# Optimization experiments

Measured on AMD Instinct MI355X. Metric: run time of the kernel, lower is better.

The kernel has to match this reference:

```python
import jax, jax.numpy as jnp
import numpy as np

B, S, D, H = 2, 2048, 2048, 16
DH = D // H            # 128 head dim
QP = D // 2            # 1024 compressed q dim
KVP = (2 * D) // 3     # 1365 compressed kv dim
RD = DH // 2           # 64 rope dim
ND = DH // 2           # 64 nope dim
FF = 4 * D
THETA = 10000.0


def _ln(x, w, b, eps=1e-5):
    m = jnp.mean(x, -1, keepdims=True)
    v = jnp.mean((x - m) ** 2, -1, keepdims=True)
    return (x - m) * jax.lax.rsqrt(v + eps) * w + b


def _rotate_half(x):
    x1, x2 = jnp.split(x, 2, axis=-1)
    return jnp.concatenate([-x2, x1], axis=-1)


def setup_inputs() -> dict:
    key = jax.random.key(0)
    ks = jax.random.split(key, 9)
    rn = lambda k, shp, s: (s * jax.random.normal(k, shp)).astype(jnp.float32)
    return {
        'x': jax.random.normal(ks[0], (B, S, D), jnp.float32),
        'attn_norm_w': jnp.ones((D,), jnp.float32), 'attn_norm_b': jnp.zeros((D,), jnp.float32),
        'W_dq': rn(ks[1], (D, QP), 0.01),
        'q_ln_w': jnp.ones((QP,), jnp.float32), 'q_ln_b': jnp.zeros((QP,), jnp.float32),
        'W_uq': rn(ks[2], (QP, D), 0.01),
        'W_dkv': rn(ks[3], (D, KVP + RD), 0.01),
        'kv_ln_w': jnp.ones((KVP,), jnp.float32), 'kv_ln_b': jnp.zeros((KVP,), jnp.float32),
        'W_ukv': rn(ks[4], (KVP, D + H * ND), 0.01),
        'W_o': rn(ks[5], (D, D), 0.01),
        'ff_norm_w': jnp.ones((D,), jnp.float32), 'ff_norm_b': jnp.zeros((D,), jnp.float32),
        'W1': rn(ks[6], (D, FF), 0.02), 'b1': jnp.zeros((FF,), jnp.float32),
        'W2': rn(ks[7], (FF, D), 0.02), 'b2': jnp.zeros((D,), jnp.float32),
    }


def reference(x, attn_norm_w, attn_norm_b, W_dq, q_ln_w, q_ln_b, W_uq, W_dkv,
              kv_ln_w, kv_ln_b, W_ukv, W_o, ff_norm_w, ff_norm_b, W1, b1, W2, b2):
    # ---- pre-LN attention ----
    h = _ln(x, attn_norm_w, attn_norm_b)
    # Q path: down-proj, LN, up-proj
    cq = _ln(h @ W_dq, q_ln_w, q_ln_b)                      # [B,S,QP]
    Q = (cq @ W_uq).reshape(B, S, H, DH).transpose(0, 2, 1, 3)  # [B,H,S,DH]
    Qn, Qr = Q[..., :ND], Q[..., ND:]
    # RoPE tables: emb [S, DH/2]; take first RD/2 freqs, tile -> [1,1,S,RD]
    pos = jnp.arange(S, dtype=jnp.float32)
    freqs = 1.0 / (THETA ** (jnp.arange(0, DH, 2, dtype=jnp.float32) / DH))
    emb = pos[:, None] * freqs[None, :]
    cos = jnp.tile(jnp.cos(emb)[:, :RD // 2], (1, 2))[None, None]
    sin = jnp.tile(jnp.sin(emb)[:, :RD // 2], (1, 2))[None, None]
    Qr = Qr * cos + _rotate_half(Qr) * sin
    # KV path: joint down-proj, split latent / shared rope key
    ckv = h @ W_dkv                                          # [B,S,KVP+RD]
    kv_lora, k_rope = ckv[..., :KVP], ckv[..., KVP:]
    kv_lora = _ln(kv_lora, kv_ln_w, kv_ln_b)
    KV = (kv_lora @ W_ukv).reshape(B, S, H, DH + ND).transpose(0, 2, 1, 3)
    K, V = KV[..., :ND], KV[..., ND:]                        # K [B,H,S,ND], V [B,H,S,DH]
    Kr = k_rope[:, None]                                     # [B,1,S,RD] shared across heads
    Kr = Kr * cos + _rotate_half(Kr) * sin
    Kr = jnp.broadcast_to(Kr, (B, H, S, RD))
    q = jnp.concatenate([Qn, Qr], -1)                        # [B,H,S,DH]
    k = jnp.concatenate([K, Kr], -1)                         # [B,H,S,DH]
    scores = jnp.einsum('bhqd,bhkd->bhqk', q, k) / jnp.sqrt(jnp.float32(DH))
    mask = jnp.tril(jnp.ones((S, S), bool))
    scores = jnp.where(mask, scores, jnp.finfo(scores.dtype).min)
    attn = jax.nn.softmax(scores, axis=-1)
    o = jnp.einsum('bhqk,bhkd->bhqd', attn, V).transpose(0, 2, 1, 3).reshape(B, S, D)
    o = o @ W_o.T
    x = x + o  # dropout is identity at eval
    # ---- pre-LN MLP ----
    r = x
    h = _ln(x, ff_norm_w, ff_norm_b)
    h = jax.nn.gelu(h @ W1 + b1, approximate=False) @ W2 + b2
    return r + h, ckv
```

## Files before the change

kernel.cpp:

```cpp
#include <hip/hip_runtime.h>
#include <hip/hip_bf16.h>
#include <math.h>

#define B_ 2
#define S_ 2048
#define D_ 2048
#define H_ 16
#define DH_ 128
#define QP_ 1024
#define KVP_ 1365
#define RD_ 64
#define ND_ 64
#define FF_ 8192
#define T_ (B_*S_)
#define CKW_ (KVP_+RD_)
#define KVW_ 3072
#define KVP_PAD 1408
#define CKW_PAD 1536

typedef __attribute__((ext_vector_type(8))) short short8;
typedef __attribute__((ext_vector_type(4))) short sh4;
typedef __attribute__((ext_vector_type(4))) float floatx4;

__device__ __forceinline__ void gload_lds16(const __hip_bfloat16* g, __hip_bfloat16* l) {
    __builtin_amdgcn_global_load_lds((const __attribute__((address_space(1))) void*)g,
                                     (__attribute__((address_space(3))) void*)l, 16, 0, 0);
}
__device__ __forceinline__ short f2bs(float f) {
    __hip_bfloat16 h = __float2bfloat16(f);
    return *reinterpret_cast<short*>(&h);
}
__device__ __forceinline__ int sw(int row, int g) { return row * 64 + ((g ^ (row & 7)) << 3); }

__device__ __forceinline__ float fast_gelu(float v) {
    float x = v * 0.70710678118654752f;
    float ax = fabsf(x);
    float t = __builtin_amdgcn_rcpf(1.f + 0.3275911f * ax);
    float y = t * (0.254829592f + t * (-0.284496736f + t * (1.421413741f + t * (-1.453152027f + t * 1.061405429f))));
    float e = __expf(-ax * ax);
    float erfv = 1.f - y * e;
    erfv = copysignf(erfv, x);
    return 0.5f * v * (1.f + erfv);
}

__global__ __launch_bounds__(256) void ln_bf16(const float* __restrict__ in, int in_stride,
                                               const float* __restrict__ w, const float* __restrict__ bb,
                                               __hip_bfloat16* __restrict__ out, int out_stride, int N)
{
    int row = blockIdx.x;
    const float* ip = in + (size_t)row * in_stride;
    __hip_bfloat16* op = out + (size_t)row * out_stride;
    int tid = threadIdx.x;
    __shared__ float s1[256], s2[256];
    float sum = 0.f, sq = 0.f;
    bool vec = (((in_stride | N | out_stride) & 3) == 0);
    if (vec) {
        const float4* ip4 = (const float4*)ip;
        int n4 = N >> 2;
        for (int i = tid; i < n4; i += 256) {
            float4 v = ip4[i];
            sum += v.x + v.y + v.z + v.w;
            sq  += v.x * v.x + v.y * v.y + v.z * v.z + v.w * v.w;
        }
        s1[tid] = sum; s2[tid] = sq; __syncthreads();
        for (int s = 128; s > 0; s >>= 1) {
            if (tid < s) { s1[tid] += s1[tid + s]; s2[tid] += s2[tid + s]; }
            __syncthreads();
        }
        float mean = s1[0] / N;
        float var  = s2[0] / N - mean * mean;
        float rstd = rsqrtf(var + 1e-5f);
        const float4* w4 = (const float4*)w;
        const float4* b4 = (const float4*)bb;
        for (int i = tid; i < n4; i += 256) {
            float4 v = ip4[i], wv = w4[i], bv = b4[i];
            sh4 o;
            o[0] = f2bs((v.x - mean) * rstd * wv.x + bv.x);
            o[1] = f2bs((v.y - mean) * rstd * wv.y + bv.y);
            o[2] = f2bs((v.z - mean) * rstd * wv.z + bv.z);
            o[3] = f2bs((v.w - mean) * rstd * wv.w + bv.w);
            *(sh4*)&op[i * 4] = o;
        }
    } else {
        for (int i = tid; i < N; i += 256) { float v = ip[i]; sum += v; sq += v * v; }
        s1[tid] = sum; s2[tid] = sq; __syncthreads();
        for (int s = 128; s > 0; s >>= 1) {
            if (tid < s) { s1[tid] += s1[tid + s]; s2[tid] += s2[tid + s]; }
            __syncthreads();
        }
        float mean = s1[0] / N;
        float var  = s2[0] / N - mean * mean;
        float rstd = rsqrtf(var + 1e-5f);
        for (int i = tid; i < N; i += 256) {
            float v = ip[i];
            op[i] = __float2bfloat16((v - mean) * rstd * w[i] + bb[i]);
        }
    }
    for (int i = N + tid; i < out_stride; i += 256) op[i] = __float2bfloat16(0.f);
}

__global__ __launch_bounds__(256) void transpose_cvt(const float* __restrict__ W, __hip_bfloat16* __restrict__ Wt,
                                                     int K, int N, int Kp)
{
    __shared__ float t[32][33];
    int k0 = blockIdx.x * 32, n0 = blockIdx.y * 32;
    int tx = threadIdx.x & 31, ty = threadIdx.x >> 5;
    for (int r = ty; r < 32; r += 8) {
        int k = k0 + r, n = n0 + tx;
        t[r][tx] = (k < K && n < N) ? W[(size_t)k * N + n] : 0.f;
    }
    __syncthreads();
    for (int r = ty; r < 32; r += 8) {
        int n = n0 + r, k = k0 + tx;
        Wt[(size_t)n * Kp + k] = __float2bfloat16(t[tx][r]);
    }
}

__global__ __launch_bounds__(256) void cvt_bf16(const float* __restrict__ in, __hip_bfloat16* __restrict__ out, int n)
{
    int i = blockIdx.x * 256 + threadIdx.x;
    if (i < n) out[i] = __float2bfloat16(in[i]);
}

template<int EPI, typename CT>
__global__ __launch_bounds__(256) void gemm_bf16(const __hip_bfloat16* __restrict__ A,
                                                 const __hip_bfloat16* __restrict__ Bt,
                                                 CT* __restrict__ C, int M, int N, int Kp, int ldc,
                                                 const float* __restrict__ bias,
                                                 const float* __restrict__ resid)
{
    __shared__ __hip_bfloat16 As[128 * 64];
    __shared__ __hip_bfloat16 Bs[128 * 64];
    int tid = threadIdx.x;
    int gx = gridDim.x;
    int nwg = gx * gridDim.y;
    int o = blockIdx.y * gx + blockIdx.x;
    int sId = ((nwg & 7) == 0) ? ((o & 7) * (nwg >> 3) + (o >> 3)) : o;
    int bm = (sId / gx) * 128;
    int bn = (sId % gx) * 128;
    int wid = tid >> 6, lane = tid & 63;
    int wm = (wid >> 1) * 64, wn = (wid & 1) * 64;
    int lrow = lane & 15;
    int quad = lane >> 4;

    floatx4 acc[4][4];
    #pragma unroll
    for (int i = 0; i < 4; ++i)
        #pragma unroll
        for (int j = 0; j < 4; ++j)
            acc[i][j] = (floatx4){0.f, 0.f, 0.f, 0.f};

    for (int k0 = 0; k0 < Kp; k0 += 64) {
        #pragma unroll
        for (int it = 0; it < 4; ++it) {
            int chunk = it * 256 + tid;
            int row = chunk >> 3, g = chunk & 7;
            int col = (g ^ (row & 7)) << 3;
            gload_lds16(A + (size_t)(bm + row) * Kp + k0 + col, &As[chunk * 8]);
        }
        #pragma unroll
        for (int it = 0; it < 4; ++it) {
            int chunk = it * 256 + tid;
            int row = chunk >> 3, g = chunk & 7;
            int col = (g ^ (row & 7)) << 3;
            gload_lds16(Bt + (size_t)(bn + row) * Kp + k0 + col, &Bs[chunk * 8]);
        }
        __syncthreads();
        #pragma unroll
        for (int kk = 0; kk < 2; ++kk) {
            short8 a[4], b[4];
            #pragma unroll
            for (int i = 0; i < 4; ++i)
                a[i] = *(const short8*)&As[sw(wm + i * 16 + lrow, kk * 4 + quad)];
            #pragma unroll
            for (int j = 0; j < 4; ++j)
                b[j] = *(const short8*)&Bs[sw(wn + j * 16 + lrow, kk * 4 + quad)];
            #pragma unroll
            for (int i = 0; i < 4; ++i)
                #pragma unroll
                for (int j = 0; j < 4; ++j)
                    acc[i][j] = __builtin_amdgcn_mfma_f32_16x16x32_bf16(a[i], b[j], acc[i][j], 0, 0, 0);
        }
        __syncthreads();
    }

    int cq4 = quad * 4;
    #pragma unroll
    for (int i = 0; i < 4; ++i) {
        #pragma unroll
        for (int j = 0; j < 4; ++j) {
            int col = bn + wn + j * 16 + lrow;
            if (col >= N) continue;
            #pragma unroll
            for (int r = 0; r < 4; ++r) {
                int rowg = bm + wm + i * 16 + cq4 + r;
                float v = acc[i][j][r];
                size_t idx = (size_t)rowg * ldc + col;
                if (EPI == 1) v += resid[idx];
                if (EPI == 2) { v += bias[col]; v = fast_gelu(v); }
                if (EPI == 3) { v += bias[col]; v += ((const float*)C)[idx]; }
                C[idx] = (CT)v;
            }
        }
    }
}

#define BARP() __builtin_amdgcn_s_barrier()
#define SCBP() __builtin_amdgcn_sched_barrier(0)
#define GATEP(nw) asm volatile("s_waitcnt vmcnt(" #nw ")" ::: "memory")

template<int EPI, typename CT>
__global__ __launch_bounds__(512, 1) void gemm_pp(const __hip_bfloat16* __restrict__ A,
                                                  const __hip_bfloat16* __restrict__ Bt,
                                                  CT* __restrict__ C, int M, int N, int Kp, int ldc,
                                                  const float* __restrict__ bias,
                                                  const float* __restrict__ resid)
{
    __shared__ __hip_bfloat16 As[3][16384];
    __shared__ __hip_bfloat16 Bs[3][8192];

    int tid = threadIdx.x;
    int wid = tid >> 6, lane = tid & 63;
    int lrow = lane & 15, quad = lane >> 4;
    int awm = (wid >> 1) * 64;
    int bwn = (wid & 1) * 64;

    int gx = gridDim.x;
    int nwg = gx * gridDim.y;
    int o = blockIdx.y * gx + blockIdx.x;
    int q8 = nwg >> 3, r8 = nwg & 7;
    int xcd = o & 7, oi = o >> 3;
    int s = (xcd < r8 ? xcd * (q8 + 1) : r8 * (q8 + 1) + (xcd - r8) * q8) + oi;
    int bm = (s / gx) * 256, bn = (s % gx) * 128;

    const __hip_bfloat16* Abm = A  + (size_t)bm * Kp;
    const __hip_bfloat16* Bbn = Bt + (size_t)bn * Kp;

    int drow = tid >> 3;
    int csw  = ((tid & 7) ^ (drow & 7)) << 3;
    int ldst = tid * 8;

#define PSTAGE_A(k0v, dst) do { \
    gload_lds16(Abm + (size_t)drow * Kp + (k0v) + csw,         (dst) + ldst); \
    gload_lds16(Abm + (size_t)(drow + 64) * Kp + (k0v) + csw,  (dst) + 4096 + ldst); \
    gload_lds16(Abm + (size_t)(drow + 128) * Kp + (k0v) + csw, (dst) + 8192 + ldst); \
    gload_lds16(Abm + (size_t)(drow + 192) * Kp + (k0v) + csw, (dst) + 12288 + ldst); \
  } while (0)
#define PSTAGE_B(k0v, dst) do { \
    gload_lds16(Bbn + (size_t)drow * Kp + (k0v) + csw,        (dst) + ldst); \
    gload_lds16(Bbn + (size_t)(drow + 64) * Kp + (k0v) + csw, (dst) + 4096 + ldst); \
  } while (0)

    int k0off = ((quad       ^ (lrow & 7)) << 3);
    int k1off = (((4 + quad) ^ (lrow & 7)) << 3);

    short8 af0[4], af1[4], bf0[4], bf1[4];
    floatx4 acc[4][4];
    #pragma unroll
    for (int m = 0; m < 4; ++m)
        #pragma unroll
        for (int n = 0; n < 4; ++n)
            acc[m][n] = (floatx4){0.f, 0.f, 0.f, 0.f};

#define PREAD(bufA, bufB, dA, dB, koff) do { \
    _Pragma("unroll") \
    for (int m = 0; m < 4; ++m) \
      dA[m] = *(const short8*)((bufA) + (awm + m * 16 + lrow) * 64 + (koff)); \
    _Pragma("unroll") \
    for (int n = 0; n < 4; ++n) \
      dB[n] = *(const short8*)((bufB) + (bwn + n * 16 + lrow) * 64 + (koff)); \
  } while (0)

#define PMFMA(fa, fb) do { \
    __builtin_amdgcn_s_setprio(1); \
    _Pragma("unroll") \
    for (int m = 0; m < 4; ++m) \
      _Pragma("unroll") \
      for (int n = 0; n < 4; ++n) \
        acc[m][n] = __builtin_amdgcn_mfma_f32_16x16x32_bf16(fa[m], fb[n], acc[m][n], 0, 0, 0); \
    __builtin_amdgcn_s_setprio(0); \
  } while (0)

    __hip_bfloat16 *aC = &As[0][0], *aN = &As[1][0], *aS = &As[2][0];
    __hip_bfloat16 *bC = &Bs[0][0], *bN = &Bs[1][0], *bS = &Bs[2][0];

    int NT = Kp >> 6;

    PSTAGE_A(0, aC);  PSTAGE_B(0, bC);
    PSTAGE_A(64, aN); PSTAGE_B(64, bN);
    GATEP(6); SCBP(); BARP(); SCBP();
    PREAD(aC, bC, af0, bf0, k0off);

    #pragma unroll 1
    for (int t = 0; t < NT; ++t) {
        int ks = ((t + 2 < NT) ? t + 2 : NT - 1) << 6;
        PSTAGE_A(ks, aS); PSTAGE_B(ks, bS);
        PREAD(aC, bC, af1, bf1, k1off);
        PMFMA(af0, bf0);
        GATEP(6); SCBP(); BARP(); SCBP();
        PREAD(aN, bN, af0, bf0, k0off);
        PMFMA(af1, bf1);
        SCBP(); BARP(); SCBP();
        __hip_bfloat16* ta = aC; aC = aN; aN = aS; aS = ta;
        __hip_bfloat16* tb = bC; bC = bN; bN = bS; bS = tb;
    }
    asm volatile("s_waitcnt vmcnt(0)" ::: "memory");

    int cq4 = quad * 4;
    #pragma unroll
    for (int m = 0; m < 4; ++m) {
        int rowg = bm + awm + m * 16 + cq4;
        #pragma unroll
        for (int n = 0; n < 4; ++n) {
            int col = bn + bwn + n * 16 + lrow;
            #pragma unroll
            for (int r = 0; r < 4; ++r) {
                float v = acc[m][n][r];
                size_t idx = (size_t)(rowg + r) * ldc + col;
                if (EPI == 1) v += resid[idx];
                if (EPI == 2) { v += bias[col]; v = fast_gelu(v); }
                if (EPI == 3) { v += bias[col]; v += ((const float*)C)[idx]; }
                C[idx] = (CT)v;
            }
        }
    }
#undef PSTAGE_A
#undef PSTAGE_B
#undef PREAD
#undef PMFMA
}

__global__ __launch_bounds__(256) void rope_q_kernel(float* __restrict__ Q)
{
    int idx = blockIdx.x * 256 + threadIdx.x;
    int i = idx & 31;
    int h = (idx >> 5) & (H_ - 1);
    int t = idx >> 9;
    float f = expf(-(float)i * (9.210340371976184f / 64.0f));
    float ang = (float)(t & (S_ - 1)) * f;
    float sv, cv; sincosf(ang, &sv, &cv);
    float* p = Q + (size_t)t * D_ + h * DH_ + ND_;
    float u = p[i], v = p[i + 32];
    p[i]      = u * cv - v * sv;
    p[i + 32] = v * cv + u * sv;
}

__global__ __launch_bounds__(256) void rope_kr_bf(const float* __restrict__ ckv, __hip_bfloat16* __restrict__ kr)
{
    int idx = blockIdx.x * 256 + threadIdx.x;
    int i = idx & 31;
    int t = idx >> 5;
    float f = expf(-(float)i * (9.210340371976184f / 64.0f));
    float ang = (float)(t & (S_ - 1)) * f;
    float sv, cv; sincosf(ang, &sv, &cv);
    const float* src = ckv + (size_t)t * CKW_ + KVP_;
    float u = src[i], v = src[i + 32];
    kr[(size_t)t * RD_ + i]      = __float2bfloat16(u * cv - v * sv);
    kr[(size_t)t * RD_ + i + 32] = __float2bfloat16(v * cv + u * sv);
}

__global__ __launch_bounds__(256) void vt_pack(const __hip_bfloat16* __restrict__ kvu,
                                               __hip_bfloat16* __restrict__ Vt)
{
    int bh = blockIdx.y; int b = bh >> 4, h = bh & 15;
    int v = threadIdx.x & 127;
    int tg = blockIdx.x * 2 + (threadIdx.x >> 7);
    int t0 = tg * 8;
    short8 o;
    #pragma unroll
    for (int j = 0; j < 8; ++j) {
        __hip_bfloat16 e = kvu[(size_t)(b * S_ + t0 + j) * KVW_ + h * 192 + 64 + v];
        o[j] = *reinterpret_cast<short*>(&e);
    }
    *(short8*)&Vt[((size_t)bh * 128 + v) * S_ + t0] = o;
}

__global__ __launch_bounds__(256) void attn_mfma(const float* __restrict__ Q,
                                                 const __hip_bfloat16* __restrict__ KVU,
                                                 const __hip_bfloat16* __restrict__ KR,
                                                 const __hip_bfloat16* __restrict__ VT,
                                                 __hip_bfloat16* __restrict__ O)
{
    __shared__ __hip_bfloat16 Kls[64 * 64];
    __shared__ __hip_bfloat16 Krls[64 * 64];
    __shared__ __hip_bfloat16 Vls[128 * 64];
    __shared__ __hip_bfloat16 Pls[4 * 32 * 64];

    int tid = threadIdx.x, wid = tid >> 6, lane = tid & 63;
    int lrow = lane & 15, quad = lane >> 4;
    int kq8 = quad * 8;
    int o = blockIdx.y * 16 + blockIdx.x;
    int sId = (o & 7) * 64 + (o >> 3);
    int qtile = 15 - (sId & 15);
    int bh = sId >> 4;
    int b = bh >> 4, h = bh & 15;
    int q0 = qtile * 128, wq = wid * 32;

    const float scale = 0.08838834764831845f;

    short8 bq[2][2], bqr[2][2];
    #pragma unroll
    for (int n = 0; n < 2; ++n) {
        const float* qrow = Q + (size_t)(b * S_ + q0 + wq + n * 16 + lrow) * D_ + h * DH_;
        #pragma unroll
        for (int s = 0; s < 2; ++s) {
            int base = s * 32 + kq8;
            #pragma unroll
            for (int j = 0; j < 8; ++j) {
                bq[n][s][j]  = f2bs(qrow[base + j] * scale);
                bqr[n][s][j] = f2bs(qrow[64 + base + j] * scale);
            }
        }
    }

    float mstate[2] = {-INFINITY, -INFINITY};
    float lstate[2] = {0.f, 0.f};
    floatx4 acco[8][2];
    #pragma unroll
    for (int vt = 0; vt < 8; ++vt)
        #pragma unroll
        for (int n = 0; n < 2; ++n)
            acco[vt][n] = (floatx4){0.f, 0.f, 0.f, 0.f};

    int nk = qtile * 2 + 2;
    int qmax_w = q0 + wq + 31;

    for (int kt = 0; kt < nk; ++kt) {
        int k0 = kt * 64;
        #pragma unroll
        for (int it = 0; it < 2; ++it) {
            int c = it * 256 + tid;
            int row = c >> 3, g = c & 7;
            int col = ((g ^ (row & 7)) << 3);
            gload_lds16(KVU + (size_t)(b * S_ + k0 + row) * KVW_ + h * 192 + col, &Kls[c * 8]);
            gload_lds16(KR + (size_t)(b * S_ + k0 + row) * RD_ + col, &Krls[c * 8]);
        }
        #pragma unroll
        for (int it = 0; it < 4; ++it) {
            int c = it * 256 + tid;
            int row = c >> 3, g = c & 7;
            int col = ((g ^ (row & 7)) << 3);
            gload_lds16(VT + ((size_t)bh * 128 + row) * S_ + k0 + col, &Vls[c * 8]);
        }
        __syncthreads();

        if (k0 <= qmax_w) {
            floatx4 sacc[4][2];
            #pragma unroll
            for (int m = 0; m < 4; ++m)
                #pragma unroll
                for (int n = 0; n < 2; ++n)
                    sacc[m][n] = (floatx4){0.f, 0.f, 0.f, 0.f};
            #pragma unroll
            for (int m = 0; m < 4; ++m) {
                short8 ak[2], akr[2];
                #pragma unroll
                for (int s = 0; s < 2; ++s) {
                    ak[s]  = *(const short8*)&Kls[sw(m * 16 + lrow, s * 4 + quad)];
                    akr[s] = *(const short8*)&Krls[sw(m * 16 + lrow, s * 4 + quad)];
                }
                #pragma unroll
                for (int n = 0; n < 2; ++n)
                    #pragma unroll
                    for (int s = 0; s < 2; ++s) {
                        sacc[m][n] = __builtin_amdgcn_mfma_f32_16x16x32_bf16(ak[s],  bq[n][s],  sacc[m][n], 0, 0, 0);
                        sacc[m][n] = __builtin_amdgcn_mfma_f32_16x16x32_bf16(akr[s], bqr[n][s], sacc[m][n], 0, 0, 0);
                    }
            }
            #pragma unroll
            for (int n = 0; n < 2; ++n) {
                int qg = q0 + wq + n * 16 + lrow;
                float tmax = -INFINITY;
                #pragma unroll
                for (int m = 0; m < 4; ++m)
                    #pragma unroll
                    for (int r = 0; r < 4; ++r) {
                        int kg = k0 + m * 16 + quad * 4 + r;
                        if (kg > qg) sacc[m][n][r] = -1e30f;
                        tmax = fmaxf(tmax, sacc[m][n][r]);
                    }
                tmax = fmaxf(tmax, __shfl_xor(tmax, 16));
                tmax = fmaxf(tmax, __shfl_xor(tmax, 32));
                float mnew = fmaxf(mstate[n], tmax);
                float alpha = __expf(mstate[n] - mnew);
                mstate[n] = mnew;
                float ps = 0.f;
                #pragma unroll
                for (int m = 0; m < 4; ++m) {
                    sh4 pk;
                    #pragma unroll
                    for (int r = 0; r < 4; ++r) {
                        float p = __expf(sacc[m][n][r] - mnew);
                        ps += p;
                        pk[r] = f2bs(p);
                    }
                    int qloc = n * 16 + lrow;
                    int off = wid * 2048 + qloc * 64 + (((m * 2 + (quad >> 1)) ^ (lrow & 7)) << 3) + ((quad & 1) << 2);
                    *(sh4*)&Pls[off] = pk;
                }
                ps += __shfl_xor(ps, 16);
                ps += __shfl_xor(ps, 32);
                lstate[n] = lstate[n] * alpha + ps;
                #pragma unroll
                for (int vt = 0; vt < 8; ++vt)
                    #pragma unroll
                    for (int r = 0; r < 4; ++r)
                        acco[vt][n][r] *= alpha;
            }
            short8 bp[2][2];
            #pragma unroll
            for (int n = 0; n < 2; ++n)
                #pragma unroll
                for (int s = 0; s < 2; ++s)
                    bp[n][s] = *(const short8*)&Pls[wid * 2048 + sw(n * 16 + lrow, s * 4 + quad)];
            #pragma unroll
            for (int vt = 0; vt < 8; ++vt) {
                short8 av[2];
                #pragma unroll
                for (int s = 0; s < 2; ++s)
                    av[s] = *(const short8*)&Vls[sw(vt * 16 + lrow, s * 4 + quad)];
                #pragma unroll
                for (int n = 0; n < 2; ++n)
                    #pragma unroll
                    for (int s = 0; s < 2; ++s)
                        acco[vt][n] = __builtin_amdgcn_mfma_f32_16x16x32_bf16(av[s], bp[n][s], acco[vt][n], 0, 0, 0);
            }
        }
        __syncthreads();
    }

    #pragma unroll
    for (int n = 0; n < 2; ++n) {
        float inv = 1.0f / lstate[n];
        int tok = b * S_ + q0 + wq + n * 16 + lrow;
        #pragma unroll
        for (int vt = 0; vt < 8; ++vt) {
            sh4 o4;
            #pragma unroll
            for (int r = 0; r < 4; ++r) o4[r] = f2bs(acco[vt][n][r] * inv);
            *(sh4*)&O[(size_t)tok * D_ + h * DH_ + vt * 16 + quad * 4] = o4;
        }
    }
}

extern "C" void kernel_launch(void* const* d_in, const int* in_sizes, int n_in,
                              void* d_out, int out_size, void* d_ws, size_t ws_size,
                              hipStream_t stream)
{
    const float* x     = (const float*)d_in[0];
    const float* anw   = (const float*)d_in[1];
    const float* anb   = (const float*)d_in[2];
    const float* W_dq  = (const float*)d_in[3];
    const float* qlw   = (const float*)d_in[4];
    const float* qlb   = (const float*)d_in[5];
    const float* W_uq  = (const float*)d_in[6];
    const float* W_dkv = (const float*)d_in[7];
    const float* kvlw  = (const float*)d_in[8];
    const float* kvlb  = (const float*)d_in[9];
    const float* W_ukv = (const float*)d_in[10];
    const float* W_o   = (const float*)d_in[11];
    const float* fnw   = (const float*)d_in[12];
    const float* fnb   = (const float*)d_in[13];
    const float* W1    = (const float*)d_in[14];
    const float* b1    = (const float*)d_in[15];
    const float* W2    = (const float*)d_in[16];
    const float* b2    = (const float*)d_in[17];

    float* out0 = (float*)d_out;
    float* ckv  = out0 + (size_t)T_ * D_;

    float* ws = (float*)d_ws;
    float* Q  = ws;
    float* cq = Q + (size_t)T_ * D_;
    __hip_bfloat16* kvu_bf = (__hip_bfloat16*)(cq + (size_t)T_ * QP_);
    __hip_bfloat16* kr_bf  = kvu_bf + (size_t)T_ * KVW_;
    __hip_bfloat16* Vt     = kr_bf + (size_t)T_ * RD_;
    __hip_bfloat16* h_bf   = Vt + (size_t)T_ * D_;
    __hip_bfloat16* cq_bf  = h_bf + (size_t)T_ * D_;
    __hip_bfloat16* kvl_bf = cq_bf + (size_t)T_ * QP_;
    __hip_bfloat16* o_bf   = kvl_bf + (size_t)T_ * KVP_PAD;
    __hip_bfloat16* wdq_t  = o_bf + (size_t)T_ * D_;
    __hip_bfloat16* wuq_t  = wdq_t + (size_t)QP_ * D_;
    __hip_bfloat16* wdkv_t = wuq_t + (size_t)D_ * QP_;
    __hip_bfloat16* wukv_t = wdkv_t + (size_t)CKW_PAD * D_;
    __hip_bfloat16* wo_b   = wukv_t + (size_t)KVW_ * KVP_PAD;
    __hip_bfloat16* w1_t   = wo_b + (size_t)D_ * D_;
    __hip_bfloat16* w2_t   = w1_t + (size_t)FF_ * D_;
    __hip_bfloat16* ff1_bf = (__hip_bfloat16*)ws;

    dim3 blk(256);
    dim3 blk8(512);

    { dim3 g(D_ / 32, QP_ / 32);       transpose_cvt<<<g, blk, 0, stream>>>(W_dq,  wdq_t,  D_, QP_, D_); }
    { dim3 g(QP_ / 32, D_ / 32);       transpose_cvt<<<g, blk, 0, stream>>>(W_uq,  wuq_t,  QP_, D_, QP_); }
    { dim3 g(D_ / 32, CKW_PAD / 32);   transpose_cvt<<<g, blk, 0, stream>>>(W_dkv, wdkv_t, D_, CKW_, D_); }
    { dim3 g(KVP_PAD / 32, KVW_ / 32); transpose_cvt<<<g, blk, 0, stream>>>(W_ukv, wukv_t, KVP_, KVW_, KVP_PAD); }
    { int n = D_ * D_;                 cvt_bf16<<<(n + 255) / 256, blk, 0, stream>>>(W_o, wo_b, n); }
    { dim3 g(D_ / 32, FF_ / 32);       transpose_cvt<<<g, blk, 0, stream>>>(W1, w1_t, D_, FF_, D_); }
    { dim3 g(FF_ / 32, D_ / 32);       transpose_cvt<<<g, blk, 0, stream>>>(W2, w2_t, FF_, D_, FF_); }

    ln_bf16<<<T_, blk, 0, stream>>>(x, D_, anw, anb, h_bf, D_, D_);
    { dim3 g(QP_ / 128, T_ / 128);
      gemm_bf16<0, float><<<g, blk, 0, stream>>>(h_bf, wdq_t, cq, T_, QP_, D_, QP_, nullptr, nullptr); }
    ln_bf16<<<T_, blk, 0, stream>>>(cq, QP_, qlw, qlb, cq_bf, QP_, QP_);
    { dim3 g(D_ / 128, T_ / 256);
      gemm_pp<0, float><<<g, blk8, 0, stream>>>(cq_bf, wuq_t, Q, T_, D_, QP_, D_, nullptr, nullptr); }
    rope_q_kernel<<<(T_ * H_ * 32) / 256, blk, 0, stream>>>(Q);
    { dim3 g(CKW_PAD / 128, T_ / 128);
      gemm_bf16<0, float><<<g, blk, 0, stream>>>(h_bf, wdkv_t, ckv, T_, CKW_, D_, CKW_, nullptr, nullptr); }
    ln_bf16<<<T_, blk, 0, stream>>>(ckv, CKW_, kvlw, kvlb, kvl_bf, KVP_PAD, KVP_);
    { dim3 g(KVW_ / 128, T_ / 256);
      gemm_pp<0, __hip_bfloat16><<<g, blk8, 0, stream>>>(kvl_bf, wukv_t, kvu_bf, T_, KVW_, KVP_PAD, KVW_, nullptr, nullptr); }
    rope_kr_bf<<<(T_ * 32) / 256, blk, 0, stream>>>(ckv, kr_bf);
    { dim3 g(S_ / 16, B_ * H_);
      vt_pack<<<g, blk, 0, stream>>>(kvu_bf, Vt); }
    { dim3 g(16, B_ * H_);
      attn_mfma<<<g, blk, 0, stream>>>(Q, kvu_bf, kr_bf, Vt, o_bf); }
    { dim3 g(D_ / 128, T_ / 256);
      gemm_pp<1, float><<<g, blk8, 0, stream>>>(o_bf, wo_b, out0, T_, D_, D_, D_, nullptr, x); }
    ln_bf16<<<T_, blk, 0, stream>>>(out0, D_, fnw, fnb, h_bf, D_, D_);
    { dim3 g(FF_ / 128, T_ / 256);
      gemm_pp<2, __hip_bfloat16><<<g, blk8, 0, stream>>>(h_bf, w1_t, ff1_bf, T_, FF_, D_, FF_, b1, nullptr); }
    { dim3 g(D_ / 128, T_ / 256);
      gemm_pp<3, float><<<g, blk8, 0, stream>>>(ff1_bf, w2_t, out0, T_, D_, FF_, D_, b2, nullptr); }
}
```

Baseline: 999.1 us.

## Add 256x256-tile GEMM with triple-buffered A, use split-K for W2

Adds a new GEMM kernel with 256x256 output tiles per 512-thread block, triple-buffered A and double-buffered B in LDS, XCD-aware block remapping, and an optional split-K via grid z. It is used for the KV up-projection and FF1. FF2 now runs as a two-way split-K into a scratch buffer (reusing the Vt region), followed by a reduction kernel that adds the bias and residual. The larger tiles are meant to raise arithmetic intensity and cut global traffic, and split-K keeps enough blocks in flight for the narrow W2 output. The cost is heavy register and LDS use (one block per CU), plus extra fp32 traffic for the partial sums.

```diff
diff --git a/kernel.cpp b/kernel.cpp
--- a/kernel.cpp
+++ b/kernel.cpp
@@ -328,6 +328,151 @@
 #undef PSTAGE_B
 #undef PREAD
 #undef PMFMA
+}
+
+template<int EPI, typename CT>
+__global__ __launch_bounds__(512, 1) void gemm_pp2(const __hip_bfloat16* __restrict__ A,
+                                                   const __hip_bfloat16* __restrict__ Bt,
+                                                   CT* __restrict__ C, int M, int N, int Klen,
+                                                   int lda, int ldb, int ldc,
+                                                   const float* __restrict__ bias,
+                                                   const float* __restrict__ resid)
+{
+    __shared__ __hip_bfloat16 As[3][16384];
+    __shared__ __hip_bfloat16 Bs[2][16384];
+
+    int tid = threadIdx.x;
+    int wid = tid >> 6, lane = tid & 63;
+    int lrow = lane & 15, quad = lane >> 4;
+    int awm = (wid >> 2) * 128;
+    int bwn = (wid & 3) * 64;
+
+    int gx = gridDim.x;
+    int nwg = gx * gridDim.y;
+    int o = blockIdx.y * gx + blockIdx.x;
+    int q8 = nwg >> 3, r8 = nwg & 7;
+    int xcd = o & 7, oi = o >> 3;
+    int s = (xcd < r8 ? xcd * (q8 + 1) : r8 * (q8 + 1) + (xcd - r8) * q8) + oi;
+    int bm = (s / gx) * 256, bn = (s % gx) * 256;
+    int koff = blockIdx.z * Klen;
+    C += (size_t)blockIdx.z * M * ldc;
+
+    const __hip_bfloat16* Abm = A  + (size_t)bm * lda + koff;
+    const __hip_bfloat16* Bbn = Bt + (size_t)bn * ldb + koff;
+
+    int drow = tid >> 3;
+    int csw  = ((tid & 7) ^ (drow & 7)) << 3;
+    int ldst = tid * 8;
+
+#define P2STAGE(base, ld, k0v, dst) do { \
+    gload_lds16((base) + (size_t)drow * (ld) + (k0v) + csw,         (dst) + ldst); \
+    gload_lds16((base) + (size_t)(drow + 64) * (ld) + (k0v) + csw,  (dst) + 4096 + ldst); \
+    gload_lds16((base) + (size_t)(drow + 128) * (ld) + (k0v) + csw, (dst) + 8192 + ldst); \
+    gload_lds16((base) + (size_t)(drow + 192) * (ld) + (k0v) + csw, (dst) + 12288 + ldst); \
+  } while (0)
+
+    int k0off = ((quad       ^ (lrow & 7)) << 3);
+    int k1off = (((4 + quad) ^ (lrow & 7)) << 3);
+
+    short8 af0[8], af1[8], bf[4];
+    floatx4 acc[8][4];
+    #pragma unroll
+    for (int m = 0; m < 8; ++m)
+        #pragma unroll
+        for (int n = 0; n < 4; ++n)
+            acc[m][n] = (floatx4){0.f, 0.f, 0.f, 0.f};
+
+#define P2READ_A(buf, dst, kof) do { \
+    _Pragma("unroll") \
+    for (int m = 0; m < 8; ++m) \
+      dst[m] = *(const short8*)((buf) + (awm + m * 16 + lrow) * 64 + (kof)); \
+  } while (0)
+#define P2READ_B(buf, kof) do { \
+    _Pragma("unroll") \
+    for (int n = 0; n < 4; ++n) \
+      bf[n] = *(const short8*)((buf) + (bwn + n * 16 + lrow) * 64 + (kof)); \
+  } while (0)
+#define P2MFMA(fa) do { \
+    __builtin_amdgcn_s_setprio(1); \
+    _Pragma("unroll") \
+    for (int m = 0; m < 8; ++m) \
+      _Pragma("unroll") \
+      for (int n = 0; n < 4; ++n) \
+        acc[m][n] = __builtin_amdgcn_mfma_f32_16x16x32_bf16(fa[m], bf[n], acc[m][n], 0, 0, 0); \
+    __builtin_amdgcn_s_setprio(0); \
+  } while (0)
+
+    __hip_bfloat16 *aC = &As[0][0], *aN = &As[1][0], *aS = &As[2][0];
+
+    int NT = Klen >> 6;
+
+    P2STAGE(Abm, lda, 0,  aC);
+    P2STAGE(Bbn, ldb, 0,  &Bs[0][0]);
+    P2STAGE(Abm, lda, 64, aN);
+    GATEP(4); SCBP(); BARP(); SCBP();
+    P2READ_A(aC, af0, k0off);
+
+    #pragma unroll 1
+    for (int t = 0; t < NT; ++t) {
+        int kA = ((t + 2 < NT) ? t + 2 : NT - 1) << 6;
+        int kB = ((t + 1 < NT) ? t + 1 : NT - 1) << 6;
+        __hip_bfloat16* bR = &Bs[t & 1][0];
+        __hip_bfloat16* bT = &Bs[(t + 1) & 1][0];
+        P2STAGE(Abm, lda, kA, aS);
+        P2STAGE(Bbn, ldb, kB, bT);
+        GATEP(8); SCBP(); BARP(); SCBP();
+        P2READ_B(bR, k0off);
+        P2READ_A(aC, af1, k1off);
+        P2MFMA(af0);
+        P2READ_B(bR, k1off);
+        P2READ_A(aN, af0, k0off);
+        P2MFMA(af1);
+        SCBP(); BARP(); SCBP();
+        __hip_bfloat16* ta = aC; aC = aN; aN = aS; aS = ta;
+    }
+    asm volatile("s_waitcnt vmcnt(0)" ::: "memory");
+
+    int cq4 = quad * 4;
+    #pragma unroll
+    for (int m = 0; m < 8; ++m) {
+        int rowg = bm + awm + m * 16 + cq4;
+        #pragma unroll
+        for (int n = 0; n < 4; ++n) {
+            int col = bn + bwn + n * 16 + lrow;
+            #pragma unroll
+            for (int r = 0; r < 4; ++r) {
+                float v = acc[m][n][r];
+                size_t idx = (size_t)(rowg + r) * ldc + col;
+                if (EPI == 1) v += resid[idx];
+                if (EPI == 2) { v += bias[col]; v = fast_gelu(v); }
+                if (EPI == 3) { v += bias[col]; v += ((const float*)C)[idx]; }
+                C[idx] = (CT)v;
+            }
+        }
+    }
+#undef P2STAGE
+#undef P2READ_A
+#undef P2READ_B
+#undef P2MFMA
+}
+
+__global__ __launch_bounds__(256) void reduce_w2(float* __restrict__ out0,
+                                                 const float* __restrict__ P,
+                                                 const float* __restrict__ b2)
+{
+    const float4* P0 = (const float4*)P;
+    const float4* P1 = (const float4*)(P + (size_t)T_ * D_);
+    const float4* bv = (const float4*)b2;
+    float4* o4 = (float4*)out0;
+    int n4 = (T_ * D_) >> 2;
+    for (int i = blockIdx.x * 256 + threadIdx.x; i < n4; i += gridDim.x * 256) {
+        float4 a = P0[i], b = P1[i], c = o4[i], d = bv[i & ((D_ >> 2) - 1)];
+        c.x += a.x + b.x + d.x;
+        c.y += a.y + b.y + d.y;
+        c.z += a.z + b.z + d.z;
+        c.w += a.w + b.w + d.w;
+        o4[i] = c;
+    }
 }
 
 __global__ __launch_bounds__(256) void rope_q_kernel(float* __restrict__ Q)
@@ -587,6 +732,7 @@
     __hip_bfloat16* w1_t   = wo_b + (size_t)D_ * D_;
     __hip_bfloat16* w2_t   = w1_t + (size_t)FF_ * D_;
     __hip_bfloat16* ff1_bf = (__hip_bfloat16*)ws;
+    float* Pw2 = (float*)Vt;
 
     dim3 blk(256);
     dim3 blk8(512);
@@ -609,8 +755,9 @@
     { dim3 g(CKW_PAD / 128, T_ / 128);
       gemm_bf16<0, float><<<g, blk, 0, stream>>>(h_bf, wdkv_t, ckv, T_, CKW_, D_, CKW_, nullptr, nullptr); }
     ln_bf16<<<T_, blk, 0, stream>>>(ckv, CKW_, kvlw, kvlb, kvl_bf, KVP_PAD, KVP_);
-    { dim3 g(KVW_ / 128, T_ / 256);
-      gemm_pp<0, __hip_bfloat16><<<g, blk8, 0, stream>>>(kvl_bf, wukv_t, kvu_bf, T_, KVW_, KVP_PAD, KVW_, nullptr, nullptr); }
+    { dim3 g(KVW_ / 256, T_ / 256);
+      gemm_pp2<0, __hip_bfloat16><<<g, blk8, 0, stream>>>(kvl_bf, wukv_t, kvu_bf, T_, KVW_,
+                                                          KVP_PAD, KVP_PAD, KVP_PAD, KVW_, nullptr, nullptr); }
     rope_kr_bf<<<(T_ * 32) / 256, blk, 0, stream>>>(ckv, kr_bf);
     { dim3 g(S_ / 16, B_ * H_);
       vt_pack<<<g, blk, 0, stream>>>(kvu_bf, Vt); }
@@ -619,8 +766,11 @@
     { dim3 g(D_ / 128, T_ / 256);
       gemm_pp<1, float><<<g, blk8, 0, stream>>>(o_bf, wo_b, out0, T_, D_, D_, D_, nullptr, x); }
     ln_bf16<<<T_, blk, 0, stream>>>(out0, D_, fnw, fnb, h_bf, D_, D_);
-    { dim3 g(FF_ / 128, T_ / 256);
-      gemm_pp<2, __hip_bfloat16><<<g, blk8, 0, stream>>>(h_bf, w1_t, ff1_bf, T_, FF_, D_, FF_, b1, nullptr); }
-    { dim3 g(D_ / 128, T_ / 256);
-      gemm_pp<3, float><<<g, blk8, 0, stream>>>(ff1_bf, w2_t, out0, T_, D_, FF_, D_, b2, nullptr); }
-}
+    { dim3 g(FF_ / 256, T_ / 256);
+      gemm_pp2<2, __hip_bfloat16><<<g, blk8, 0, stream>>>(h_bf, w1_t, ff1_bf, T_, FF_,
+                                                          D_, D_, D_, FF_, b1, nullptr); }
+    { dim3 g(D_ / 256, T_ / 256, 2);
+      gemm_pp2<0, float><<<g, blk8, 0, stream>>>(ff1_bf, w2_t, Pw2, T_, D_,
+                                                 FF_ / 2, FF_, FF_, D_, nullptr, nullptr); }
+    reduce_w2<<<1024, blk, 0, stream>>>(out0, Pw2, b2);
+}
```

New measurement: 1.029 ms. +3.0%, slower.
